# Performance work log

Measured on AMD Instinct MI355X. Metric: run time of the kernel, lower is better.

Reference implementation:

```python
import jax, jax.numpy as jnp
import numpy as np

B = 16
H_DIM = 512
N_HEADS = 8
HEAD_DIM = H_DIM // N_HEADS  # 64
EPS = 1e-5
DST_LENS = 256 + 16 * np.arange(B)  # ragged dst sizes, total 6016
SRC_LENS = 512 - 8 * np.arange(B)   # ragged src sizes, total 7232


def _pad_info(lens):
    # gather/scatter indices to move between flat ragged layout and [B, Lmax, D]
    lens = np.asarray(lens)
    off = np.concatenate([[0], np.cumsum(lens)[:-1]])
    gid = np.repeat(np.arange(len(lens)), lens)
    pos = np.arange(int(lens.sum())) - np.repeat(off, lens)
    Lmax = int(lens.max())
    mask = jnp.asarray(np.arange(Lmax)[None, :] < lens[:, None])
    return gid, pos, Lmax, mask


def _bn(x, g, b):
    # BatchNorm1d forward with batch statistics (training-mode normalization)
    m = x.mean(0)
    v = ((x - m) ** 2).mean(0)
    return (x - m) / jnp.sqrt(v + EPS) * g + b


def setup_inputs() -> dict:
    key = jax.random.key(0)
    ks = jax.random.split(key, 20)
    total_src = int(SRC_LENS.sum())
    total_dst = int(DST_LENS.sum())
    w = lambda k, shape: jax.random.normal(k, shape, jnp.float32) * 0.02
    return {
        "src_h": jax.random.normal(ks[0], (total_src, H_DIM), jnp.float32),
        "dst_h": jax.random.normal(ks[1], (total_dst, H_DIM), jnp.float32),
        "src_num_verts": jnp.asarray(SRC_LENS, jnp.int32),
        "dst_num_verts": jnp.asarray(DST_LENS, jnp.int32),
        "Wq": w(ks[2], (H_DIM, H_DIM)), "bq": w(ks[3], (H_DIM,)),
        "Wk": w(ks[4], (H_DIM, H_DIM)), "bk": w(ks[5], (H_DIM,)),
        "Wv": w(ks[6], (H_DIM, H_DIM)), "bv": w(ks[7], (H_DIM,)),
        "Wm": w(ks[8], (H_DIM, H_DIM)), "bm": w(ks[9], (H_DIM,)),
        "W1": w(ks[10], (H_DIM, 2 * H_DIM)), "b1": w(ks[11], (H_DIM,)),
        "g1": jnp.ones((H_DIM,), jnp.float32), "be1": jnp.zeros((H_DIM,), jnp.float32),
        "W2": w(ks[12], (H_DIM, H_DIM)), "b2": w(ks[13], (H_DIM,)),
        "g2": jnp.ones((H_DIM,), jnp.float32), "be2": jnp.zeros((H_DIM,), jnp.float32),
    }


def reference(src_h, dst_h, src_num_verts, dst_num_verts,
              Wq, bq, Wk, bk, Wv, bv, Wm, bm,
              W1, b1, g1, be1, W2, b2, g2, be2):
    s_lens = np.asarray(src_num_verts)
    d_lens = np.asarray(dst_num_verts)
    sg, sp, Ls, smask = _pad_info(s_lens)
    dg, dp, Ld, dmask = _pad_info(d_lens)

    # ragged -> padded [B, L, D]
    src_pad = jnp.zeros((B, Ls, H_DIM), src_h.dtype).at[sg, sp].set(src_h)
    dst_pad = jnp.zeros((B, Ld, H_DIM), dst_h.dtype).at[dg, dp].set(dst_h)

    # Conv1d(k=1) projections; channel c = d*num_heads + h -> reshape (head_dim, n_heads)
    q = (dst_pad @ Wq.T + bq).reshape(B, Ld, HEAD_DIM, N_HEADS)
    k = (src_pad @ Wk.T + bk).reshape(B, Ls, HEAD_DIM, N_HEADS)
    v = (src_pad @ Wv.T + bv).reshape(B, Ls, HEAD_DIM, N_HEADS)

    scores = jnp.einsum('bndh,bmdh->bhnm', q, k) / 8.0  # sqrt(head_dim)=8
    scores = jnp.where(smask[:, None, None, :], scores, -1e9)
    attn = jax.nn.softmax(scores, axis=-1)
    o = jnp.einsum('bhnm,bmdh->bndh', attn, v).reshape(B, Ld, H_DIM)
    o = o @ Wm.T + bm  # merge Conv1d(k=1)

    # padded -> ragged
    h_msg = o[dg, dp]  # [total_dst, h_dim]

    h = dst_h
    x = jnp.concatenate([h, h_msg], axis=-1)
    x = _bn(x @ W1.T + b1, g1, be1)
    x = jax.nn.relu(x)
    x = _bn(x @ W2.T + b2, g2, be2)
    return h + x
```

## Files before the change

### kernel.cpp

```cpp
#include <hip/hip_runtime.h>
#include <hip/hip_bf16.h>

#define H_DIM 512
#define N_HEADS 8
#define HEAD_DIM 64
#define NBATCH 16

typedef __attribute__((ext_vector_type(8))) short short8;
typedef __attribute__((ext_vector_type(4))) float floatx4;

typedef unsigned short us16;

#define SW3(r) ((((r) >> 1) & 3) | (((r) & 1) << 2))

#define PERMC(c) ((((c) & 7) << 6) | ((c) >> 3))
#define IPERMC(cp) ((((cp) & 63) << 3) | ((cp) >> 6))

__device__ inline unsigned short f2bf(float f) {
  unsigned int u = __float_as_uint(f);
  unsigned int r = (u + 0x7fffu + ((u >> 16) & 1u)) >> 16;
  return (unsigned short)r;
}

__device__ inline void gld16(const us16* g, us16* l) {
  __builtin_amdgcn_global_load_lds(
      (const __attribute__((address_space(1))) void*)g,
      (__attribute__((address_space(3))) void*)l, 16, 0, 0);
}

__global__ __launch_bounds__(256) void prep_all(
    const float* __restrict__ src_h, const float* __restrict__ dst_h,
    const float* __restrict__ Wq, const float* __restrict__ Wk,
    const float* __restrict__ Wv, const float* __restrict__ W1,
    const float* __restrict__ W2, const float* __restrict__ Wm,
    const float* __restrict__ b1, const float* __restrict__ bm,
    us16* __restrict__ src_bf, us16* __restrict__ dst_bf,
    us16* __restrict__ Wqb, us16* __restrict__ Wkv, us16* __restrict__ Wf,
    us16* __restrict__ W2b, float* __restrict__ b1p, float* __restrict__ st,
    int n_src, int n_dst) {
  __shared__ __align__(16) us16 As[64 * 48];
  __shared__ __align__(16) us16 Bs[64 * 48];
  const int blk = blockIdx.x;
  const int t = threadIdx.x;

  if (blk < 2048) {
    if (blk == 0) {
      float4 z = make_float4(0.f, 0.f, 0.f, 0.f);
      ((float4*)st)[t] = z;
      ((float4*)st)[t + 256] = z;
    }
    const float* srcs[7] = {src_h, dst_h, Wq, Wk, Wv, W1, W2};
    us16* dsts[7] = {src_bf, dst_bf, Wqb, Wkv, Wkv + 262144, Wf, W2b};
    int ns[7] = {n_src, n_dst, 262144, 262144, 262144, 262144, 262144};
    const int md_[7] = {0, 0, 2, 2, 0, 1, 0};
    for (int rg = 0; rg < 7; ++rg) {
      const float* sp = srcs[rg];
      us16* dp = dsts[rg];
      const int mode = md_[rg];
      for (int i = (blk * 256 + t) * 4; i < ns[rg]; i += 2048 * 256 * 4) {
        int js, jd;
        if (mode == 1) {
          js = ((i >> 9) * 1024) + (i & 511);
          jd = js;
        } else if (mode == 2) {
          int r = i >> 9;
          js = i;
          jd = (PERMC(r) << 9) + (i & 511);
        } else {
          js = i; jd = i;
        }
        float4 v = *(const float4*)(sp + js);
        ushort4 o;
        o.x = f2bf(v.x); o.y = f2bf(v.y); o.z = f2bf(v.z); o.w = f2bf(v.w);
        *(ushort4*)(dp + jd) = o;
      }
    }
  } else if (blk < 2112) {
    const int bx = (blk - 2048) & 7, byk = (blk - 2048) >> 3;
    const int w = t >> 6, lane = t & 63;
    const int lane15 = lane & 15, quad = lane >> 4;
    const int wm = w >> 1, wn = w & 1;
    const int bn_ = bx * 64, bk = byk * 64;
    floatx4 acc[2][2];
#pragma unroll
    for (int a = 0; a < 2; ++a)
#pragma unroll
      for (int c = 0; c < 2; ++c) acc[a][c] = (floatx4){0.f, 0.f, 0.f, 0.f};
    for (int j0 = 0; j0 < 512; j0 += 32) {
      {
        int n = t >> 2, jj0 = (t & 3) * 8;
        const float* rp = W1 + (size_t)(bn_ + n) * 1024 + 512 + j0 + jj0;
        float4 va = *(const float4*)(rp);
        float4 vb = *(const float4*)(rp + 4);
        ushort4 pa, pb;
        pa.x = f2bf(va.x); pa.y = f2bf(va.y); pa.z = f2bf(va.z); pa.w = f2bf(va.w);
        pb.x = f2bf(vb.x); pb.y = f2bf(vb.y); pb.z = f2bf(vb.z); pb.w = f2bf(vb.w);
        *(ushort4*)(As + n * 48 + jj0) = pa;
        *(ushort4*)(As + n * 48 + jj0 + 4) = pb;
      }
      {
        int jj = t >> 3, kc0 = (t & 7) * 8;
        const float* rp = Wm + (size_t)(j0 + jj) * 512 + bk + kc0;
        float4 va = *(const float4*)(rp);
        float4 vb = *(const float4*)(rp + 4);
        float vv[8] = {va.x, va.y, va.z, va.w, vb.x, vb.y, vb.z, vb.w};
#pragma unroll
        for (int e = 0; e < 8; ++e) Bs[(kc0 + e) * 48 + jj] = f2bf(vv[e]);
      }
      __syncthreads();
      short8 a_[2], b_[2];
#pragma unroll
      for (int mt = 0; mt < 2; ++mt)
        a_[mt] = *(const short8*)(As + (wm * 32 + mt * 16 + lane15) * 48 + quad * 8);
#pragma unroll
      for (int nt = 0; nt < 2; ++nt)
        b_[nt] = *(const short8*)(Bs + (wn * 32 + nt * 16 + lane15) * 48 + quad * 8);
#pragma unroll
      for (int mt = 0; mt < 2; ++mt)
#pragma unroll
        for (int nt = 0; nt < 2; ++nt)
          acc[mt][nt] = __builtin_amdgcn_mfma_f32_16x16x32_bf16(
              a_[mt], b_[nt], acc[mt][nt], 0, 0, 0);
      __syncthreads();
    }
#pragma unroll
    for (int mt = 0; mt < 2; ++mt) {
      int n0 = bn_ + wm * 32 + mt * 16 + quad * 4;
#pragma unroll
      for (int nt = 0; nt < 2; ++nt) {
        int k = bk + wn * 32 + nt * 16 + lane15;
        int kp = PERMC(k);
#pragma unroll
        for (int r = 0; r < 4; ++r)
          Wf[(size_t)(n0 + r) * 1024 + 512 + kp] = f2bf(acc[mt][nt][r]);
      }
    }
  } else {
    int n = (blk - 2112) * 256 + t;
    if (n < 512) {
      const float* rp = W1 + (size_t)n * 1024 + 512;
      float s = 0.f;
      for (int j = 0; j < 512; j += 4) {
        float4 a = *(const float4*)(rp + j);
        float4 c = *(const float4*)(bm + j);
        s += a.x * c.x + a.y * c.y + a.z * c.z + a.w * c.w;
      }
      b1p[n] = b1[n] + s;
    }
  }
}

__device__ inline void gemm_body(
    const us16* __restrict__ A1, const us16* __restrict__ A2,
    const us16* __restrict__ W,
    const float* __restrict__ bias0, const float* __restrict__ bias1,
    void* __restrict__ C0, void* __restrict__ C1, float* __restrict__ stats,
    int M, int N, int K, int mode, int bx, int by) {
  __shared__ __align__(16) us16 As[2 * 64 * 64];
  __shared__ __align__(16) us16 Bs[2 * 128 * 64];
  const int t = threadIdx.x, w = t >> 6, lane = t & 63;
  const int lane15 = lane & 15, quad = lane >> 4;
  const int bm = bx * 64, bn = by * 128;
  const int lrow = lane >> 3;
  const int sl = lane & 7;

  floatx4 acc[4][2];
#pragma unroll
  for (int a = 0; a < 4; ++a)
#pragma unroll
    for (int c = 0; c < 2; ++c) acc[a][c] = (floatx4){0.f, 0.f, 0.f, 0.f};

  const int nk = K >> 6;

#define ISSUE(i, b)                                                          \
  {                                                                          \
    int k0 = (i) << 6;                                                       \
    const us16* Ab = (k0 < 512) ? A1 : A2;                                   \
    int ka = k0 & 511;                                                       \
    _Pragma("unroll")                                                        \
    for (int p = 0; p < 2; ++p) {                                            \
      int rbase = p * 32 + w * 8;                                            \
      int row = rbase + lrow;                                                \
      int kg = sl ^ SW3(row);                                                \
      gld16(Ab + (size_t)(bm + row) * 512 + ka + kg * 8,                     \
            As + (b) * 4096 + rbase * 64);                                   \
    }                                                                        \
    _Pragma("unroll")                                                        \
    for (int p = 0; p < 4; ++p) {                                            \
      int rbase = p * 32 + w * 8;                                            \
      int row = rbase + lrow;                                                \
      int kg = sl ^ SW3(row);                                                \
      gld16(W + (size_t)(bn + row) * K + k0 + kg * 8,                        \
            Bs + (b) * 8192 + rbase * 64);                                   \
    }                                                                        \
  }

  ISSUE(0, 0);
  if (nk > 1) ISSUE(1, 1);
  for (int i = 0; i < nk; ++i) {
    const int cur = i & 1;
    if (i + 1 < nk) {
      asm volatile("s_waitcnt vmcnt(6)" ::: "memory");
    } else {
      asm volatile("s_waitcnt vmcnt(0)" ::: "memory");
    }
    __builtin_amdgcn_s_barrier();
    asm volatile("" ::: "memory");
#pragma unroll
    for (int kh = 0; kh < 2; ++kh) {
      const int g = kh * 4 + quad;
      short8 a_[4], b_[2];
#pragma unroll
      for (int mt = 0; mt < 4; ++mt) {
        int r = mt * 16 + lane15;
        a_[mt] = *(const short8*)(As + cur * 4096 + r * 64 + (g ^ SW3(r)) * 8);
      }
#pragma unroll
      for (int nt = 0; nt < 2; ++nt) {
        int c = w * 32 + nt * 16 + lane15;
        b_[nt] = *(const short8*)(Bs + cur * 8192 + c * 64 + (g ^ SW3(c)) * 8);
      }
#pragma unroll
      for (int mt = 0; mt < 4; ++mt)
#pragma unroll
        for (int nt = 0; nt < 2; ++nt)
          acc[mt][nt] = __builtin_amdgcn_mfma_f32_16x16x32_bf16(
              a_[mt], b_[nt], acc[mt][nt], 0, 0, 0);
    }
    asm volatile("" ::: "memory");
    __builtin_amdgcn_s_barrier();
    asm volatile("" ::: "memory");
    if (i + 2 < nk) ISSUE(i + 2, cur);
  }
#undef ISSUE

  if (mode == 0) {
#pragma unroll
    for (int nt = 0; nt < 2; ++nt) {
      int col = bn + w * 32 + nt * 16 + lane15;
      float bv = bias0[col];
      float s = 0.f, qq = 0.f;
#pragma unroll
      for (int mt = 0; mt < 4; ++mt) {
        int row0 = bm + mt * 16 + quad * 4;
#pragma unroll
        for (int r = 0; r < 4; ++r) {
          float val = acc[mt][nt][r] + bv;
          ((float*)C0)[(size_t)(row0 + r) * N + col] = val;
          s += val; qq = fmaf(val, val, qq);
        }
      }
      s += __shfl_xor(s, 16); s += __shfl_xor(s, 32);
      qq += __shfl_xor(qq, 16); qq += __shfl_xor(qq, 32);
      if (quad == 0) {
        atomicAdd(&stats[col], s);
        atomicAdd(&stats[512 + col], qq);
      }
    }
  } else if (mode == 1) {
#pragma unroll
    for (int nt = 0; nt < 2; ++nt) {
      int col = bn + w * 32 + nt * 16 + lane15;
      float bv = bias0[IPERMC(col)];
#pragma unroll
      for (int mt = 0; mt < 4; ++mt) {
        int row0 = bm + mt * 16 + quad * 4;
#pragma unroll
        for (int r = 0; r < 4; ++r)
          ((us16*)C0)[(size_t)(row0 + r) * 512 + col] = f2bf(acc[mt][nt][r] + bv);
      }
    }
  } else {
#pragma unroll
    for (int nt = 0; nt < 2; ++nt) {
      int col = bn + w * 32 + nt * 16 + lane15;
      if (col < 512) {
        float bv = bias0[IPERMC(col)];
#pragma unroll
        for (int mt = 0; mt < 4; ++mt) {
          int row0 = bm + mt * 16 + quad * 4;
#pragma unroll
          for (int r = 0; r < 4; ++r)
            ((us16*)C0)[(size_t)(row0 + r) * 512 + col] = f2bf(acc[mt][nt][r] + bv);
        }
      } else {
        int cv = col - 512;
        float bv = bias1[cv];
        int plane = (cv & 7) * 64 + (cv >> 3);
#pragma unroll
        for (int mt = 0; mt < 4; ++mt) {
          int row0 = bm + mt * 16 + quad * 4;
          ushort4 pk;
          pk.x = f2bf(acc[mt][nt][0] + bv);
          pk.y = f2bf(acc[mt][nt][1] + bv);
          pk.z = f2bf(acc[mt][nt][2] + bv);
          pk.w = f2bf(acc[mt][nt][3] + bv);
          *(ushort4*)((us16*)C1 + (size_t)plane * M + row0) = pk;
        }
      }
    }
  }
}

__global__ __launch_bounds__(256) void gemm_ffn(
    const us16* __restrict__ A1, const us16* __restrict__ A2,
    const us16* __restrict__ W,
    const float* __restrict__ bias0, void* __restrict__ C0,
    float* __restrict__ stats, int M, int K) {
  int b = blockIdx.x;
  int i = (b & 7) * ((int)gridDim.x >> 3) + (b >> 3);
  gemm_body(A1, A2, W, bias0, nullptr, C0, nullptr, stats, M, 512, K, 0,
            i >> 2, i & 3);
}

__global__ __launch_bounds__(256) void gemm_qkv(
    const us16* __restrict__ dst_bf, const us16* __restrict__ src_bf,
    const us16* __restrict__ Wqb, const us16* __restrict__ Wkv,
    const float* __restrict__ bq, const float* __restrict__ bk,
    const float* __restrict__ bv,
    us16* __restrict__ Qh, us16* __restrict__ Kh, us16* __restrict__ Vt,
    int Md, int Ms) {
  int b = blockIdx.x;
  int i = (b & 7) * ((int)gridDim.x >> 3) + (b >> 3);
  int nq = (Md / 64) * 4;
  if (i < nq) {
    gemm_body(dst_bf, dst_bf, Wqb, bq, nullptr, Qh, nullptr, nullptr,
              Md, 512, 512, 1, i >> 2, i & 3);
  } else {
    int j = i - nq;
    gemm_body(src_bf, src_bf, Wkv, bk, bv, Kh, Vt, nullptr,
              Ms, 1024, 512, 4, j >> 3, j & 7);
  }
}

__global__ __launch_bounds__(256) void attn_v6(
    const us16* __restrict__ Qh, const us16* __restrict__ Kh,
    const us16* __restrict__ Vt, const int* __restrict__ dlens,
    const int* __restrict__ slens, us16* __restrict__ O,
    int Md, int Ms) {
  const int b = blockIdx.x, h = blockIdx.y, tile = blockIdx.z;
  int doff = 0, soff = 0;
  for (int i = 0; i < NBATCH; ++i)
    if (i < b) { doff += dlens[i]; soff += slens[i]; }
  const int dlen = dlens[b], slen = slens[b];
  if (tile * 64 >= dlen) return;

  __shared__ __align__(16) us16 Ks[2 * 64 * 64];
  __shared__ __align__(16) us16 Vts[2 * 64 * 64];
  __shared__ __align__(16) us16 Pw[4][16 * 72];

  const int t = threadIdx.x, wv = t >> 6, lane = t & 63;
  const int lane15 = lane & 15, quad = lane >> 4;
  const int i0w = tile * 64 + wv * 16;
  const bool active = i0w < dlen;

  const us16* Qp = Qh + ((size_t)(doff + (active ? i0w : 0))) * 512 + h * 64;
  const us16* Kp = Kh + ((size_t)soff) * 512 + h * 64;
  const us16* Vtp = Vt + ((size_t)h * 64) * Ms + soff;

  short8 af0 = *(const short8*)(Qp + (size_t)lane15 * 512 + quad * 8);
  short8 af1 = *(const short8*)(Qp + (size_t)lane15 * 512 + 32 + quad * 8);

  floatx4 oa[4];
#pragma unroll
  for (int nt = 0; nt < 4; ++nt) oa[nt] = (floatx4){0.f, 0.f, 0.f, 0.f};
  float m_r[4] = {-3.0e38f, -3.0e38f, -3.0e38f, -3.0e38f};
  float l_r[4] = {0.f, 0.f, 0.f, 0.f};

  const int nc = (slen + 63) >> 6;

#define KVST(c, bu)                                                       \
  {                                                                       \
    int jb = (c) << 6;                                                    \
    _Pragma("unroll")                                                     \
    for (int p = 0; p < 2; ++p) {                                         \
      int row = wv * 16 + p * 8 + (lane >> 3);                            \
      int slt = lane & 7;                                                 \
      int kg = slt ^ SW3(row);                                            \
      gld16(Kp + (size_t)(jb + row) * 512 + kg * 8,                       \
            Ks + (bu) * 4096 + (wv * 16 + p * 8) * 64);                   \
      gld16(Vtp + (size_t)row * Ms + jb + kg * 8,                         \
            Vts + (bu) * 4096 + (wv * 16 + p * 8) * 64);                  \
    }                                                                     \
  }

  KVST(0, 0);
  if (nc > 1) KVST(1, 1);
  for (int c = 0; c < nc; ++c) {
    const int cur = c & 1;
    if (c + 1 < nc) {
      asm volatile("s_waitcnt vmcnt(4)" ::: "memory");
    } else {
      asm volatile("s_waitcnt vmcnt(0)" ::: "memory");
    }
    __builtin_amdgcn_s_barrier();
    asm volatile("" ::: "memory");

    if (active) {
      const int j0 = c << 6;
      floatx4 s[4];
#pragma unroll
      for (int jt = 0; jt < 4; ++jt) {
        int j = jt * 16 + lane15;
        short8 b0 = *(const short8*)(Ks + cur * 4096 + j * 64 + ((quad ^ SW3(j)) * 8));
        short8 b1 = *(const short8*)(Ks + cur * 4096 + j * 64 + (((4 + quad) ^ SW3(j)) * 8));
        floatx4 a = (floatx4){0.f, 0.f, 0.f, 0.f};
        a = __builtin_amdgcn_mfma_f32_16x16x32_bf16(af0, b0, a, 0, 0, 0);
        a = __builtin_amdgcn_mfma_f32_16x16x32_bf16(af1, b1, a, 0, 0, 0);
        s[jt] = a;
      }
      float mx[4] = {-3.0e38f, -3.0e38f, -3.0e38f, -3.0e38f};
#pragma unroll
      for (int jt = 0; jt < 4; ++jt) {
        bool valid = (j0 + jt * 16 + lane15) < slen;
#pragma unroll
        for (int r = 0; r < 4; ++r) {
          float v = valid ? s[jt][r] * 0.125f : -3.0e38f;
          s[jt][r] = v;
          mx[r] = fmaxf(mx[r], v);
        }
      }
#pragma unroll
      for (int r = 0; r < 4; ++r) {
        mx[r] = fmaxf(mx[r], __shfl_xor(mx[r], 1));
        mx[r] = fmaxf(mx[r], __shfl_xor(mx[r], 2));
        mx[r] = fmaxf(mx[r], __shfl_xor(mx[r], 4));
        mx[r] = fmaxf(mx[r], __shfl_xor(mx[r], 8));
      }
      float al[4], sum[4];
#pragma unroll
      for (int r = 0; r < 4; ++r) {
        float mn = fmaxf(m_r[r], mx[r]);
        al[r] = __expf(m_r[r] - mn);
        m_r[r] = mn;
        sum[r] = 0.f;
      }
#pragma unroll
      for (int jt = 0; jt < 4; ++jt)
#pragma unroll
        for (int r = 0; r < 4; ++r) {
          float e = __expf(s[jt][r] - m_r[r]);
          sum[r] += e;
          Pw[wv][(quad * 4 + r) * 72 + jt * 16 + lane15] = f2bf(e);
        }
#pragma unroll
      for (int r = 0; r < 4; ++r) {
        sum[r] += __shfl_xor(sum[r], 1);
        sum[r] += __shfl_xor(sum[r], 2);
        sum[r] += __shfl_xor(sum[r], 4);
        sum[r] += __shfl_xor(sum[r], 8);
        l_r[r] = l_r[r] * al[r] + sum[r];
      }
#pragma unroll
      for (int nt = 0; nt < 4; ++nt)
#pragma unroll
        for (int r = 0; r < 4; ++r) oa[nt][r] *= al[r];
      short8 pa0 = *(const short8*)(&Pw[wv][lane15 * 72 + quad * 8]);
      short8 pa1 = *(const short8*)(&Pw[wv][lane15 * 72 + 32 + quad * 8]);
#pragma unroll
      for (int nt = 0; nt < 4; ++nt) {
        int d = nt * 16 + lane15;
        short8 v0 = *(const short8*)(Vts + cur * 4096 + d * 64 + ((quad ^ SW3(d)) * 8));
        short8 v1 = *(const short8*)(Vts + cur * 4096 + d * 64 + (((4 + quad) ^ SW3(d)) * 8));
        oa[nt] = __builtin_amdgcn_mfma_f32_16x16x32_bf16(pa0, v0, oa[nt], 0, 0, 0);
        oa[nt] = __builtin_amdgcn_mfma_f32_16x16x32_bf16(pa1, v1, oa[nt], 0, 0, 0);
      }
    }

    asm volatile("" ::: "memory");
    __builtin_amdgcn_s_barrier();
    asm volatile("" ::: "memory");
    if (c + 2 < nc) KVST(c + 2, cur);
  }
#undef KVST

  if (active) {
    float linv[4];
#pragma unroll
    for (int r = 0; r < 4; ++r) linv[r] = 1.f / l_r[r];
#pragma unroll
    for (int r = 0; r < 4; ++r) {
      int i = quad * 4 + r;
      us16* orow = O + (size_t)(doff + i0w + i) * H_DIM + h * 64;
#pragma unroll
      for (int nt = 0; nt < 4; ++nt) {
        int d = nt * 16 + lane15;
        orow[d] = f2bf(oa[nt][r] * linv[r]);
      }
    }
  }
}

__global__ __launch_bounds__(256) void bn_apply(
    const float* __restrict__ X, const float* __restrict__ stats,
    const float* __restrict__ g, const float* __restrict__ be,
    const float* __restrict__ resid, void* __restrict__ Y,
    int M, float invM, int relu, int out_bf) {
  const size_t total = (size_t)M * H_DIM;
  for (size_t i = (size_t)blockIdx.x * 256 + threadIdx.x; i < total;
       i += (size_t)gridDim.x * 256) {
    int c = (int)(i & (H_DIM - 1));
    float mean = stats[c] * invM;
    float var = fmaf(-mean, mean, stats[H_DIM + c] * invM);
    float x = X[i];
    float y = (x - mean) * rsqrtf(var + 1e-5f) * g[c] + be[c];
    if (relu) y = fmaxf(y, 0.f);
    if (resid) y += resid[i];
    if (out_bf) ((us16*)Y)[i] = f2bf(y);
    else ((float*)Y)[i] = y;
  }
}

extern "C" void kernel_launch(void* const* d_in, const int* in_sizes, int n_in,
                              void* d_out, int out_size, void* d_ws, size_t ws_size,
                              hipStream_t stream) {
  const float* src_h = (const float*)d_in[0];
  const float* dst_h = (const float*)d_in[1];
  const int* s_lens  = (const int*)d_in[2];
  const int* d_lens  = (const int*)d_in[3];
  const float* Wq = (const float*)d_in[4];  const float* bq = (const float*)d_in[5];
  const float* Wk = (const float*)d_in[6];  const float* bk = (const float*)d_in[7];
  const float* Wv = (const float*)d_in[8];  const float* bv = (const float*)d_in[9];
  const float* Wm = (const float*)d_in[10]; const float* bm = (const float*)d_in[11];
  const float* W1 = (const float*)d_in[12]; const float* b1 = (const float*)d_in[13];
  const float* g1 = (const float*)d_in[14]; const float* be1 = (const float*)d_in[15];
  const float* W2 = (const float*)d_in[16]; const float* b2 = (const float*)d_in[17];
  const float* g2 = (const float*)d_in[18]; const float* be2 = (const float*)d_in[19];

  const int total_src = in_sizes[0] / H_DIM;
  const int total_dst = in_sizes[1] / H_DIM;

  char* ws = (char*)d_ws;
  us16* src_bf = (us16*)(ws + 0);
  us16* dst_bf = (us16*)(ws + 7405568);
  us16* wbf    = (us16*)(ws + 13565952);
  float* b1p   = (float*)(ws + 16711680);
  us16* Qh     = (us16*)(ws + 17235968);
  us16* Kh     = (us16*)(ws + 23396352);
  us16* Vt     = (us16*)(ws + 30801920);
  us16* Ob     = (us16*)(ws + 38207488);
  us16* X1bf   = (us16*)(ws + 44367872);
  float* st    = (float*)(ws + 50528256);
  float* X1    = (float*)(ws + 17235968);
  float* X2    = (float*)(ws + 30801920);
  float* st1 = st, *st2 = st + 1024;

  us16* Wqb = wbf;
  us16* Wkv = wbf + 262144;
  us16* Wf  = wbf + 786432;
  us16* W2b = wbf + 1310720;

  const int mbd = total_dst / 64;
  const int mbs = total_src / 64;
  const dim3 blk256(256);

  prep_all<<<dim3(2114), blk256, 0, stream>>>(
      src_h, dst_h, Wq, Wk, Wv, W1, W2, Wm, b1, bm,
      src_bf, dst_bf, Wqb, Wkv, Wf, W2b, b1p, st,
      total_src * H_DIM, total_dst * H_DIM);

  gemm_qkv<<<dim3(mbd * 4 + mbs * 8), blk256, 0, stream>>>(
      dst_bf, src_bf, Wqb, Wkv, bq, bk, bv, Qh, Kh, Vt, total_dst, total_src);

  attn_v6<<<dim3(NBATCH, N_HEADS, 8), blk256, 0, stream>>>(
      Qh, Kh, Vt, d_lens, s_lens, Ob, total_dst, total_src);

  gemm_ffn<<<dim3(mbd * 4), blk256, 0, stream>>>(
      dst_bf, Ob, Wf, b1p, X1, st1, total_dst, 1024);

  bn_apply<<<dim3(512), blk256, 0, stream>>>(X1, st1, g1, be1, nullptr, X1bf,
                                             total_dst, 1.f / (float)total_dst, 1, 1);

  gemm_ffn<<<dim3(mbd * 4), blk256, 0, stream>>>(
      X1bf, X1bf, W2b, b2, X2, st2, total_dst, 512);

  bn_apply<<<dim3(512), blk256, 0, stream>>>(X2, st2, g2, be2, dst_h, d_out,
                                             total_dst, 1.f / (float)total_dst, 0, 0);
}
```

Before: 237.1 us.

## Fuse first BatchNorm+ReLU into second FFN GEMM prologue, vectorize final BN

Removes the standalone BN1 apply kernel and its bf16 intermediate buffer. The new GEMM loads fp32 X1 tiles into registers, applies per-channel scale/shift and ReLU, converts to bf16 and stores into swizzled LDS, while still staging W via async loads. The final BN apply is specialized to float4 with a residual add. The trade-off is a GEMM that now reads A as fp32 (twice the bytes) with register-staged rather than direct LDS loads, which adds register pressure and ALU work inside the main loop.

```diff
diff --git a/kernel.cpp b/kernel.cpp
--- a/kernel.cpp
+++ b/kernel.cpp
@@ -333,6 +333,155 @@
   }
 }
 
+__global__ __launch_bounds__(256) void gemm_ffn2bn(
+    const float* __restrict__ X1, const us16* __restrict__ W,
+    const float* __restrict__ st1, const float* __restrict__ g1,
+    const float* __restrict__ be1, const float* __restrict__ b2,
+    float* __restrict__ X2, float* __restrict__ st2, int M, float invM) {
+  __shared__ __align__(16) us16 As[2 * 64 * 64];
+  __shared__ __align__(16) us16 Bs[2 * 128 * 64];
+  __shared__ float slt[512], tlt[512];
+  int b = blockIdx.x;
+  int i0 = (b & 7) * ((int)gridDim.x >> 3) + (b >> 3);
+  const int bx = i0 >> 2, by = i0 & 3;
+  const int t = threadIdx.x, w = t >> 6, lane = t & 63;
+  const int lane15 = lane & 15, quad = lane >> 4;
+  const int bm = bx * 64, bn = by * 128;
+  const int lrow = lane >> 3;
+  const int sl = lane & 7;
+
+  for (int c = t; c < 512; c += 256) {
+    float mean = st1[c] * invM;
+    float var = fmaf(-mean, mean, st1[512 + c] * invM);
+    float inv = rsqrtf(var + 1e-5f) * g1[c];
+    slt[c] = inv;
+    tlt[c] = be1[c] - mean * inv;
+  }
+  __syncthreads();
+
+  floatx4 acc[4][2];
+#pragma unroll
+  for (int a = 0; a < 4; ++a)
+#pragma unroll
+    for (int c = 0; c < 2; ++c) acc[a][c] = (floatx4){0.f, 0.f, 0.f, 0.f};
+
+  const int arow = t >> 2;
+  const int ac4 = (t & 3) * 16;
+  const int s0 = (t & 3) * 2;
+
+#define ALOAD(dst, ii)                                                       \
+  {                                                                          \
+    const float* p_ = X1 + (size_t)(bm + arow) * 512 + ((ii) << 6) + ac4;    \
+    dst[0] = *(const float4*)(p_);                                           \
+    dst[1] = *(const float4*)(p_ + 4);                                       \
+    dst[2] = *(const float4*)(p_ + 8);                                       \
+    dst[3] = *(const float4*)(p_ + 12);                                      \
+  }
+
+#define BISSUE(ii, bb)                                                       \
+  {                                                                          \
+    int k0 = (ii) << 6;                                                      \
+    _Pragma("unroll")                                                        \
+    for (int p = 0; p < 4; ++p) {                                            \
+      int rbase = p * 32 + w * 8;                                            \
+      int row = rbase + lrow;                                                \
+      int kg = sl ^ SW3(row);                                                \
+      gld16(W + (size_t)(bn + row) * 512 + k0 + kg * 8,                      \
+            Bs + (bb) * 8192 + rbase * 64);                                  \
+    }                                                                        \
+  }
+
+  float4 areg[2][4];
+  ALOAD(areg[0], 0);
+  BISSUE(0, 0);
+  asm volatile("" ::: "memory");
+  ALOAD(areg[1], 1);
+  BISSUE(1, 1);
+
+#pragma unroll
+  for (int i = 0; i < 8; ++i) {
+    const int cur = i & 1;
+    if (i + 1 < 8) {
+      asm volatile("s_waitcnt vmcnt(8)" ::: "memory");
+    } else {
+      asm volatile("s_waitcnt vmcnt(0)" ::: "memory");
+    }
+    {
+      const int k0 = i << 6;
+      __align__(16) us16 vv[16];
+#pragma unroll
+      for (int q = 0; q < 4; ++q) {
+#pragma unroll
+        for (int j = 0; j < 4; ++j) {
+          int c = k0 + ac4 + q * 4 + j;
+          float x = ((const float*)&areg[cur][q])[j];
+          float y = fmaxf(fmaf(x, slt[c], tlt[c]), 0.f);
+          vv[q * 4 + j] = f2bf(y);
+        }
+      }
+      us16* base = As + cur * 4096 + arow * 64;
+      *(short8*)(base + ((s0 ^ SW3(arow)) * 8)) = *(short8*)&vv[0];
+      *(short8*)(base + (((s0 + 1) ^ SW3(arow)) * 8)) = *(short8*)&vv[8];
+    }
+    asm volatile("s_waitcnt lgkmcnt(0)" ::: "memory");
+    __builtin_amdgcn_s_barrier();
+    asm volatile("" ::: "memory");
+#pragma unroll
+    for (int kh = 0; kh < 2; ++kh) {
+      const int g = kh * 4 + quad;
+      short8 a_[4], b_[2];
+#pragma unroll
+      for (int mt = 0; mt < 4; ++mt) {
+        int r = mt * 16 + lane15;
+        a_[mt] = *(const short8*)(As + cur * 4096 + r * 64 + (g ^ SW3(r)) * 8);
+      }
+#pragma unroll
+      for (int nt = 0; nt < 2; ++nt) {
+        int c = w * 32 + nt * 16 + lane15;
+        b_[nt] = *(const short8*)(Bs + cur * 8192 + c * 64 + (g ^ SW3(c)) * 8);
+      }
+#pragma unroll
+      for (int mt = 0; mt < 4; ++mt)
+#pragma unroll
+        for (int nt = 0; nt < 2; ++nt)
+          acc[mt][nt] = __builtin_amdgcn_mfma_f32_16x16x32_bf16(
+              a_[mt], b_[nt], acc[mt][nt], 0, 0, 0);
+    }
+    asm volatile("" ::: "memory");
+    __builtin_amdgcn_s_barrier();
+    asm volatile("" ::: "memory");
+    if (i + 2 < 8) {
+      ALOAD(areg[cur], i + 2);
+      BISSUE(i + 2, cur);
+    }
+  }
+#undef ALOAD
+#undef BISSUE
+
+#pragma unroll
+  for (int nt = 0; nt < 2; ++nt) {
+    int col = bn + w * 32 + nt * 16 + lane15;
+    float bv = b2[col];
+    float s = 0.f, qq = 0.f;
+#pragma unroll
+    for (int mt = 0; mt < 4; ++mt) {
+      int row0 = bm + mt * 16 + quad * 4;
+#pragma unroll
+      for (int r = 0; r < 4; ++r) {
+        float val = acc[mt][nt][r] + bv;
+        X2[(size_t)(row0 + r) * 512 + col] = val;
+        s += val; qq = fmaf(val, val, qq);
+      }
+    }
+    s += __shfl_xor(s, 16); s += __shfl_xor(s, 32);
+    qq += __shfl_xor(qq, 16); qq += __shfl_xor(qq, 32);
+    if (quad == 0) {
+      atomicAdd(&st2[col], s);
+      atomicAdd(&st2[512 + col], qq);
+    }
+  }
+}
+
 __global__ __launch_bounds__(256) void attn_v6(
     const us16* __restrict__ Qh, const us16* __restrict__ Kh,
     const us16* __restrict__ Vt, const int* __restrict__ dlens,
@@ -491,23 +640,28 @@
   }
 }
 
-__global__ __launch_bounds__(256) void bn_apply(
+__global__ __launch_bounds__(256) void bn2_apply(
     const float* __restrict__ X, const float* __restrict__ stats,
     const float* __restrict__ g, const float* __restrict__ be,
-    const float* __restrict__ resid, void* __restrict__ Y,
-    int M, float invM, int relu, int out_bf) {
-  const size_t total = (size_t)M * H_DIM;
-  for (size_t i = (size_t)blockIdx.x * 256 + threadIdx.x; i < total;
+    const float* __restrict__ resid, float* __restrict__ Y,
+    int M, float invM) {
+  const size_t total4 = (size_t)M * (H_DIM / 4);
+  for (size_t i = (size_t)blockIdx.x * 256 + threadIdx.x; i < total4;
        i += (size_t)gridDim.x * 256) {
-    int c = (int)(i & (H_DIM - 1));
-    float mean = stats[c] * invM;
-    float var = fmaf(-mean, mean, stats[H_DIM + c] * invM);
-    float x = X[i];
-    float y = (x - mean) * rsqrtf(var + 1e-5f) * g[c] + be[c];
-    if (relu) y = fmaxf(y, 0.f);
-    if (resid) y += resid[i];
-    if (out_bf) ((us16*)Y)[i] = f2bf(y);
-    else ((float*)Y)[i] = y;
+    int c = (int)((i * 4) & (H_DIM - 1));
+    float4 x = ((const float4*)X)[i];
+    float4 rr = ((const float4*)resid)[i];
+    float4 o;
+#pragma unroll
+    for (int j = 0; j < 4; ++j) {
+      int cc = c + j;
+      float mean = stats[cc] * invM;
+      float var = fmaf(-mean, mean, stats[H_DIM + cc] * invM);
+      float inv = rsqrtf(var + 1e-5f) * g[cc];
+      float xv = ((const float*)&x)[j];
+      ((float*)&o)[j] = (xv - mean) * inv + be[cc] + ((const float*)&rr)[j];
+    }
+    ((float4*)Y)[i] = o;
   }
 }
 
@@ -539,7 +693,6 @@
   us16* Kh     = (us16*)(ws + 23396352);
   us16* Vt     = (us16*)(ws + 30801920);
   us16* Ob     = (us16*)(ws + 38207488);
-  us16* X1bf   = (us16*)(ws + 44367872);
   float* st    = (float*)(ws + 50528256);
   float* X1    = (float*)(ws + 17235968);
   float* X2    = (float*)(ws + 30801920);
@@ -553,6 +706,7 @@
   const int mbd = total_dst / 64;
   const int mbs = total_src / 64;
   const dim3 blk256(256);
+  const float invM = 1.f / (float)total_dst;
 
   prep_all<<<dim3(2114), blk256, 0, stream>>>(
       src_h, dst_h, Wq, Wk, Wv, W1, W2, Wm, b1, bm,
@@ -568,12 +722,9 @@
   gemm_ffn<<<dim3(mbd * 4), blk256, 0, stream>>>(
       dst_bf, Ob, Wf, b1p, X1, st1, total_dst, 1024);
 
-  bn_apply<<<dim3(512), blk256, 0, stream>>>(X1, st1, g1, be1, nullptr, X1bf,
-                                             total_dst, 1.f / (float)total_dst, 1, 1);
-
-  gemm_ffn<<<dim3(mbd * 4), blk256, 0, stream>>>(
-      X1bf, X1bf, W2b, b2, X2, st2, total_dst, 512);
-
-  bn_apply<<<dim3(512), blk256, 0, stream>>>(X2, st2, g2, be2, dst_h, d_out,
-                                             total_dst, 1.f / (float)total_dst, 0, 0);
-}
+  gemm_ffn2bn<<<dim3(mbd * 4), blk256, 0, stream>>>(
+      X1, W2b, st1, g1, be1, b2, X2, st2, total_dst, invM);
+
+  bn2_apply<<<dim3(512), blk256, 0, stream>>>(
+      X2, st2, g2, be2, dst_h, (float*)d_out, total_dst, invM);
+}
```

After: 220.0 us. 7.2% less time.
